# Optimization experiments

Hardware: AMD Instinct MI355X
Metric: run time of the kernel (lower is better)

## Reference

```python
import jax, jax.numpy as jnp
import numpy as np

GAMMA = 1.4
N_PTS, N_IC, HID = 32768, 16384, 128


def _mlp(layers, p):
    # tanh MLP; layers = list of (W, b), last layer linear
    h = p
    for W, b in layers[:-1]:
        h = jnp.tanh(h @ W + b)
    W, b = layers[-1]
    return h @ W + b


def setup_inputs() -> dict:
    key = jax.random.key(0)
    ks = jax.random.split(key, 16)
    d = {
        "x_train": jax.random.uniform(ks[0], (N_PTS, 3), jnp.float32),
        "x_initial": jax.random.uniform(ks[1], (N_IC, 3), jnp.float32),
        "ic": jax.random.uniform(ks[2], (4, 4), jnp.float32),
    }
    def lin(k, fi, fo):
        return jax.random.normal(k, (fi, fo), jnp.float32) * np.float32(np.sqrt(1.0 / fi))
    dims_m = [(3, HID), (HID, HID), (HID, HID), (HID, 4)]
    dims_n = [(3, HID), (HID, HID), (HID, HID), (HID, 1)]
    for i, (fi, fo) in enumerate(dims_m):
        d[f"mw{i}"] = lin(ks[3 + i], fi, fo)
        d[f"mb{i}"] = jnp.zeros((fo,), jnp.float32)
    for i, (fi, fo) in enumerate(dims_n):
        d[f"nw{i}"] = lin(ks[8 + i], fi, fo)
        d[f"nb{i}"] = jnp.zeros((fo,), jnp.float32)
    return d


def _loss(x_train, x_initial, ic,
          mw0, mb0, mw1, mb1, mw2, mb2, mw3, mb3,
          nw0, nb0, nw1, nb1, nw2, nb2, nw3, nb3):
    layers_m = [(mw0, mb0), (mw1, mb1), (mw2, mb2), (mw3, mb3)]
    layers_n = [(nw0, nb0), (nw1, nb1), (nw2, nb2), (nw3, nb3)]

    def prim(p):  # p: (3,) = (x, y, t)
        o = _mlp(layers_m, p)
        rho, pr, u, v = o[0], o[1], o[2], o[3]
        E = pr / (GAMMA - 1.0) + 0.5 * rho * (u * u + v * v)
        return rho, pr, u, v, E

    def Ufn(p):  # conserved state U1..U4
        rho, pr, u, v, E = prim(p)
        return jnp.stack([rho, rho * u, rho * v, E])

    def quant(p):  # [U1..U4, f1..f4, g1..g4]
        rho, pr, u, v, E = prim(p)
        U = jnp.stack([rho, rho * u, rho * v, E])
        f = jnp.stack([rho * u, rho * u * u + pr, rho * u * v, u * (E + pr)])
        g = jnp.stack([rho * v, rho * u * v, rho * v * v + pr, v * (E + pr)])
        return jnp.concatenate([U, f, g])

    # one fused forward-mode Jacobian sweep replaces 20 torch autograd.grad calls
    J = jax.vmap(jax.jacfwd(quant))(x_train)            # (N, 12, 3)
    Hs = jax.vmap(jax.jacfwd(jax.jacfwd(Ufn)))(x_train)  # (N, 4, 3, 3)

    mu = 0.01 * jnp.squeeze(_mlp(layers_n, x_train), -1) ** 2  # (N,)
    lap = Hs[:, :, 0, 0] + Hs[:, :, 1, 1]               # U_xx + U_yy, (N, 4)
    # res_i = U_i_t + f_i_x + g_i_y - mu * (U_i_xx + U_i_yy)
    res = J[:, 0:4, 2] + J[:, 4:8, 0] + J[:, 8:12, 1] - mu[:, None] * lap
    r = jnp.mean(res ** 2, axis=0)                      # (4,) -> r1..r4

    # initial-condition quadrant loss (masked means, jit-safe)
    pred = _mlp(layers_m, x_initial)                    # (Ni, 4)
    xl = x_initial[:, 0] < 0.5
    xr = x_initial[:, 0] > 0.5
    yt = x_initial[:, 1] > 0.5
    yb = x_initial[:, 1] < 0.5
    perm = jnp.array([0, 3, 1, 2])  # ic columns -> [rho, p, u, v] target order
    init_loss = jnp.float32(0.0)
    for row, mask in ((1, xl & yt), (3, xr & yt), (0, xl & yb), (2, xr & yb)):
        tgt = ic[row][perm]                             # (4,)
        m = mask.astype(pred.dtype)
        denom = jnp.maximum(jnp.sum(m), 1.0)
        init_loss = init_loss + jnp.sum(m[:, None] * (pred - tgt) ** 2) / denom

    return jnp.sum(r) + 10.0 * init_loss + 0.1 * jnp.mean(mu ** 2)


def reference(x_train, x_initial, ic,
              mw0, mb0, mw1, mb1, mw2, mb2, mw3, mb3,
              nw0, nb0, nw1, nb1, nw2, nb2, nw3, nb3):
    return _loss(x_train, x_initial, ic,
                 mw0, mb0, mw1, mb1, mw2, mb2, mw3, mb3,
                 nw0, nb0, nw1, nb1, nw2, nb2, nw3, nb3)
```

## Files before the change

kernel.cpp:

```cpp
#include <hip/hip_runtime.h>

#define NPTS 32768
#define NIC  16384
#define GRID 256
#define GRID_MU 512
#define BLK  512
#define NW   8

typedef __attribute__((ext_vector_type(8))) _Float16 f16x8;
typedef __attribute__((ext_vector_type(4))) float f32x4;

#define SWZ(e, r) ((e) ^ (((r) & 7) << 3))
#define MFMA16 __builtin_amdgcn_mfma_f32_16x16x32_f16

__device__ __forceinline__ float tanh_fast(float x) {
    float e = __expf(2.0f * x);
    return 1.0f - 2.0f / (e + 1.0f);
}

__device__ __forceinline__ float wave_allsum(float v) {
#pragma unroll
    for (int off = 32; off > 0; off >>= 1) v += __shfl_xor(v, off, 64);
    return v;
}

__device__ __forceinline__ unsigned short f2hb(float x) {
    return __builtin_bit_cast(unsigned short, (_Float16)x);
}
__device__ __forceinline__ uint2 pack4h(float a, float b, float c, float d) {
    return make_uint2((unsigned)f2hb(a) | ((unsigned)f2hb(b) << 16),
                      (unsigned)f2hb(c) | ((unsigned)f2hb(d) << 16));
}

__global__ __launch_bounds__(BLK) void k_prep(
    const float* __restrict__ mw1, const float* __restrict__ mw2,
    const float* __restrict__ nw1, const float* __restrict__ nw2,
    const float* __restrict__ mw3,
    unsigned short* __restrict__ wt1, unsigned short* __restrict__ wt2,
    unsigned short* __restrict__ nt1, unsigned short* __restrict__ nt2,
    unsigned short* __restrict__ w3t) {
    const int tid = threadIdx.x;
    const int bk = blockIdx.x;
    if (bk == 4) {
        for (int i = tid; i < 2048; i += BLK) w3t[i] = 0;
        __syncthreads();
        if (tid < 512) {
            const int j = tid & 127, k = tid >> 7;
            w3t[k * 128 + SWZ(j, k)] = f2hb(mw3[j * 4 + k]);
        }
        return;
    }
    const float* src = (bk == 0) ? mw1 : (bk == 1) ? mw2 : (bk == 2) ? nw1 : nw2;
    unsigned short* dst = (bk == 0) ? wt1 : (bk == 1) ? wt2 : (bk == 2) ? nt1 : nt2;
    __shared__ float sM[128 * 129];
#pragma unroll
    for (int k = 0; k < 32; k++) {
        const int idx = tid + k * BLK;
        const int j = idx >> 7, n = idx & 127;
        sM[n * 129 + j] = src[idx];
    }
    __syncthreads();
#pragma unroll
    for (int k = 0; k < 32; k++) {
        const int d = tid + k * BLK;
        const int n = d >> 7, js = d & 127;
        const int j = js ^ ((n & 7) << 3);
        dst[d] = f2hb(sM[n * 129 + j]);
    }
}

__global__ __launch_bounds__(BLK) void k_residual(
    const float* __restrict__ xtr,
    const float* __restrict__ mw0, const float* __restrict__ mb0,
    const float* __restrict__ mb1, const float* __restrict__ mb2,
    const float* __restrict__ mb3,
    const unsigned short* __restrict__ wt1, const unsigned short* __restrict__ wt2,
    const unsigned short* __restrict__ w3t,
    const float* __restrict__ muArr, float* __restrict__ resPart) {
    __shared__ __align__(16) _Float16 sW1[16384];
    __shared__ __align__(16) _Float16 sW2[16384];
    __shared__ __align__(16) _Float16 sW3[2048];
    __shared__ __align__(16) _Float16 sH[6 * 4096];
    __shared__ __align__(16) float sO[6 * 32 * 4];
    __shared__ float sB[260];

    const int tid = threadIdx.x;
    const int lane = tid & 63, wv = tid >> 6;
    const int g = lane >> 4, l15 = lane & 15;
    const int rtp = wv >> 1;
    const int ptile = wv & 1;
    const int bp = ptile * 16 + l15;
    const int p32 = tid & 31;
    const int chunk = tid >> 5;

    {
        const uint4* s4 = (const uint4*)wt1;
        uint4* d4 = (uint4*)sW1;
#pragma unroll
        for (int k = 0; k < 4; k++) d4[tid + k * BLK] = s4[tid + k * BLK];
        s4 = (const uint4*)wt2; d4 = (uint4*)sW2;
#pragma unroll
        for (int k = 0; k < 4; k++) d4[tid + k * BLK] = s4[tid + k * BLK];
        if (tid < 256) ((uint4*)sW3)[tid] = ((const uint4*)w3t)[tid];
        if (tid < 128) { sB[tid] = mb1[tid]; sB[128 + tid] = mb2[tid]; }
        if (tid < 4) sB[256 + tid] = mb3[tid];
    }
    float wxr[8], wyr[8], wzr[8], wbr[8];
#pragma unroll
    for (int j = 0; j < 8; j++) {
        const int n = chunk * 8 + j;
        wxr[j] = mw0[n]; wyr[j] = mw0[128 + n]; wzr[j] = mw0[256 + n]; wbr[j] = mb0[n];
    }
    __syncthreads();

    float racc0 = 0.f, racc1 = 0.f, racc2 = 0.f, racc3 = 0.f;
    const int base = blockIdx.x * 128;

    for (int b = 0; b < 4; b++) {
        const int pt0 = base + b * 32;

        {
            const int p = pt0 + p32;
            const float x = xtr[p * 3 + 0], y = xtr[p * 3 + 1], t = xtr[p * 3 + 2];
            float ch[6][8];
#pragma unroll
            for (int j = 0; j < 8; j++) {
                const float z = fmaf(wxr[j], x, fmaf(wyr[j], y, fmaf(wzr[j], t, wbr[j])));
                const float a = tanh_fast(z);
                const float s = 1.f - a * a;
                ch[0][j] = a;
                ch[1][j] = s * wxr[j];
                ch[2][j] = s * wyr[j];
                ch[3][j] = s * wzr[j];
                ch[4][j] = -2.f * a * s * wxr[j] * wxr[j];
                ch[5][j] = -2.f * a * s * wyr[j] * wyr[j];
            }
            const int off = p32 * 128 + SWZ(chunk * 8, p32);
#pragma unroll
            for (int c = 0; c < 6; c++) {
                const uint2 lo = pack4h(ch[c][0], ch[c][1], ch[c][2], ch[c][3]);
                const uint2 hi = pack4h(ch[c][4], ch[c][5], ch[c][6], ch[c][7]);
                *(uint4*)&sH[c * 4096 + off] = make_uint4(lo.x, lo.y, hi.x, hi.y);
            }
        }
        __syncthreads();

#pragma unroll
        for (int L = 0; L < 2; L++) {
            const _Float16* W = (L == 0) ? sW1 : sW2;
            f32x4 acc[2][6];
#pragma unroll
            for (int rr = 0; rr < 2; rr++)
#pragma unroll
                for (int c = 0; c < 6; c++) acc[rr][c] = (f32x4){0.f, 0.f, 0.f, 0.f};
#pragma unroll
            for (int ks = 0; ks < 4; ks++) {
                const int ee = SWZ(ks * 32 + g * 8, l15);
                const f16x8 A0 = *(const f16x8*)&W[(rtp * 32 + l15) * 128 + ee];
                const f16x8 A1 = *(const f16x8*)&W[(rtp * 32 + 16 + l15) * 128 + ee];
#pragma unroll
                for (int c = 0; c < 6; c++) {
                    const f16x8 Bv = *(const f16x8*)&sH[c * 4096 + bp * 128 + ee];
                    acc[0][c] = MFMA16(A0, Bv, acc[0][c], 0, 0, 0);
                    acc[1][c] = MFMA16(A1, Bv, acc[1][c], 0, 0, 0);
                }
            }
            float ch[2][6][4];
#pragma unroll
            for (int rr = 0; rr < 2; rr++)
#pragma unroll
                for (int r = 0; r < 4; r++) {
                    const int n = rtp * 32 + rr * 16 + g * 4 + r;
                    const float z0 = acc[rr][0][r] + sB[L * 128 + n];
                    const float a = tanh_fast(z0);
                    const float s = 1.f - a * a;
                    const float zx = acc[rr][1][r], zy = acc[rr][2][r];
                    ch[rr][0][r] = a;
                    ch[rr][1][r] = s * zx;
                    ch[rr][2][r] = s * zy;
                    ch[rr][3][r] = s * acc[rr][3][r];
                    ch[rr][4][r] = s * acc[rr][4][r] - 2.f * a * s * zx * zx;
                    ch[rr][5][r] = s * acc[rr][5][r] - 2.f * a * s * zy * zy;
                }
            __syncthreads();
#pragma unroll
            for (int rr = 0; rr < 2; rr++) {
                const int eo = bp * 128 + SWZ(rtp * 32 + rr * 16 + g * 4, bp);
#pragma unroll
                for (int c = 0; c < 6; c++)
                    *(uint2*)&sH[c * 4096 + eo] =
                        pack4h(ch[rr][c][0], ch[rr][c][1], ch[rr][c][2], ch[rr][c][3]);
            }
            __syncthreads();
        }

#pragma unroll
        for (int tt = 0; tt < 2; tt++) {
            const int t = wv + tt * 8;
            if (t < 12) {
                const int c = t % 6, pti = t / 6;
                const int fp = pti * 16 + l15;
                f32x4 a4 = (f32x4){0.f, 0.f, 0.f, 0.f};
#pragma unroll
                for (int ks = 0; ks < 4; ks++) {
                    const int ee = SWZ(ks * 32 + g * 8, l15);
                    const f16x8 Af = *(const f16x8*)&sW3[l15 * 128 + ee];
                    const f16x8 Bf = *(const f16x8*)&sH[c * 4096 + fp * 128 + ee];
                    a4 = MFMA16(Af, Bf, a4, 0, 0, 0);
                }
                if (g == 0) {
                    float4 o = make_float4(a4[0], a4[1], a4[2], a4[3]);
                    if (c == 0) { o.x += sB[256]; o.y += sB[257]; o.z += sB[258]; o.w += sB[259]; }
                    *(float4*)&sO[(c * 32 + fp) * 4] = o;
                }
            }
        }
        __syncthreads();

        {
            const float m = muArr[pt0 + p32];
            float oq[4][6];
#pragma unroll
            for (int c = 0; c < 6; c++) {
                const float4 o = *(const float4*)&sO[(c * 32 + p32) * 4];
                oq[0][c] = o.x; oq[1][c] = o.y; oq[2][c] = o.z; oq[3][c] = o.w;
            }
            const float rho = oq[0][0], rho_x = oq[0][1], rho_y = oq[0][2],
                        rho_t = oq[0][3], rho_xx = oq[0][4], rho_yy = oq[0][5];
            const float pr = oq[1][0], pr_x = oq[1][1], pr_y = oq[1][2],
                        pr_t = oq[1][3], pr_xx = oq[1][4], pr_yy = oq[1][5];
            const float u = oq[2][0], u_x = oq[2][1], u_y = oq[2][2],
                        u_t = oq[2][3], u_xx = oq[2][4], u_yy = oq[2][5];
            const float v = oq[3][0], v_x = oq[3][1], v_y = oq[3][2],
                        v_t = oq[3][3], v_xx = oq[3][4], v_yy = oq[3][5];

            const float ig1 = 2.5f;
            const float ke = 0.5f * (u * u + v * v);
            const float E = pr * ig1 + rho * ke;
            const float d_x = u * u_x + v * v_x;
            const float d_y = u * u_y + v * v_y;
            const float d_t = u * u_t + v * v_t;
            const float E_x = pr_x * ig1 + rho_x * ke + rho * d_x;
            const float E_y = pr_y * ig1 + rho_y * ke + rho * d_y;
            const float E_t = pr_t * ig1 + rho_t * ke + rho * d_t;
            const float E_xx = pr_xx * ig1 + rho_xx * ke + 2.f * rho_x * d_x +
                               rho * (u_x * u_x + u * u_xx + v_x * v_x + v * v_xx);
            const float E_yy = pr_yy * ig1 + rho_yy * ke + 2.f * rho_y * d_y +
                               rho * (u_y * u_y + u * u_yy + v_y * v_y + v * v_yy);

            const float r1 = rho_t + (rho_x * u + rho * u_x) + (rho_y * v + rho * v_y)
                           - m * (rho_xx + rho_yy);
            const float r2 = (rho_t * u + rho * u_t)
                           + (rho_x * u * u + 2.f * rho * u * u_x + pr_x)
                           + (rho_y * u * v + rho * u_y * v + rho * u * v_y)
                           - m * ((rho_xx * u + 2.f * rho_x * u_x + rho * u_xx)
                                + (rho_yy * u + 2.f * rho_y * u_y + rho * u_yy));
            const float r3 = (rho_t * v + rho * v_t)
                           + (rho_x * u * v + rho * u_x * v + rho * u * v_x)
                           + (rho_y * v * v + 2.f * rho * v * v_y + pr_y)
                           - m * ((rho_xx * v + 2.f * rho_x * v_x + rho * v_xx)
                                + (rho_yy * v + 2.f * rho_y * v_y + rho * v_yy));
            const float r4 = E_t
                           + (u_x * (E + pr) + u * (E_x + pr_x))
                           + (v_y * (E + pr) + v * (E_y + pr_y))
                           - m * (E_xx + E_yy);
            if (tid < 32) {
                racc0 += r1 * r1; racc1 += r2 * r2;
                racc2 += r3 * r3; racc3 += r4 * r4;
            }
        }
    }

    if (wv == 0) {
        racc0 = wave_allsum(racc0);
        racc1 = wave_allsum(racc1);
        racc2 = wave_allsum(racc2);
        racc3 = wave_allsum(racc3);
        if (lane == 0) {
            resPart[blockIdx.x * 4 + 0] = racc0;
            resPart[blockIdx.x * 4 + 1] = racc1;
            resPart[blockIdx.x * 4 + 2] = racc2;
            resPart[blockIdx.x * 4 + 3] = racc3;
        }
    }
}

__global__ __launch_bounds__(BLK) void k_mu(
    const float* __restrict__ xtr,
    const float* __restrict__ nw0, const float* __restrict__ nb0,
    const float* __restrict__ nb1, const float* __restrict__ nb2,
    const float* __restrict__ nw3, const float* __restrict__ nb3,
    const unsigned short* __restrict__ nt1, const unsigned short* __restrict__ nt2,
    float* __restrict__ muArr, float* __restrict__ muPart) {
    __shared__ __align__(16) _Float16 sW1[16384];
    __shared__ __align__(16) _Float16 sW2[16384];
    __shared__ __align__(16) _Float16 sH[4096];
    __shared__ float sV[128], sB[257];
    __shared__ float sRed[NW];

    const int tid = threadIdx.x;
    const int lane = tid & 63, wv = tid >> 6;
    const int g = lane >> 4, l15 = lane & 15;
    const int rtp = wv >> 1, ptile = wv & 1;
    const int bp = ptile * 16 + l15;
    const int p32 = tid & 31;
    const int chunk = tid >> 5;

    {
        const uint4* s4 = (const uint4*)nt1;
        uint4* d4 = (uint4*)sW1;
#pragma unroll
        for (int k = 0; k < 4; k++) d4[tid + k * BLK] = s4[tid + k * BLK];
        s4 = (const uint4*)nt2; d4 = (uint4*)sW2;
#pragma unroll
        for (int k = 0; k < 4; k++) d4[tid + k * BLK] = s4[tid + k * BLK];
        if (tid < 128) { sV[tid] = nw3[tid]; sB[tid] = nb1[tid]; }
        else if (tid < 256) sB[tid] = nb2[tid - 128];
        if (tid == 256) sB[256] = nb3[0];
    }
    float wxr[8], wyr[8], wzr[8], wbr[8];
#pragma unroll
    for (int j = 0; j < 8; j++) {
        const int n = chunk * 8 + j;
        wxr[j] = nw0[n]; wyr[j] = nw0[128 + n]; wzr[j] = nw0[256 + n]; wbr[j] = nb0[n];
    }
    __syncthreads();

    float accMu2 = 0.f;

    for (int b = 0; b < 2; b++) {
        const int pt0 = blockIdx.x * 64 + b * 32;
        {
            const int p = pt0 + p32;
            const float x = xtr[p * 3 + 0], y = xtr[p * 3 + 1], t = xtr[p * 3 + 2];
            float hv[8];
#pragma unroll
            for (int j = 0; j < 8; j++)
                hv[j] = tanh_fast(fmaf(wxr[j], x, fmaf(wyr[j], y, fmaf(wzr[j], t, wbr[j]))));
            const uint2 lo = pack4h(hv[0], hv[1], hv[2], hv[3]);
            const uint2 hi = pack4h(hv[4], hv[5], hv[6], hv[7]);
            *(uint4*)&sH[p32 * 128 + SWZ(chunk * 8, p32)] = make_uint4(lo.x, lo.y, hi.x, hi.y);
        }
        __syncthreads();
#pragma unroll
        for (int L = 0; L < 2; L++) {
            const _Float16* W = (L == 0) ? sW1 : sW2;
            f32x4 acc[2];
            acc[0] = (f32x4){0.f, 0.f, 0.f, 0.f};
            acc[1] = (f32x4){0.f, 0.f, 0.f, 0.f};
#pragma unroll
            for (int ks = 0; ks < 4; ks++) {
                const int ee = SWZ(ks * 32 + g * 8, l15);
                const f16x8 A0 = *(const f16x8*)&W[(rtp * 32 + l15) * 128 + ee];
                const f16x8 A1 = *(const f16x8*)&W[(rtp * 32 + 16 + l15) * 128 + ee];
                const f16x8 Bv = *(const f16x8*)&sH[bp * 128 + ee];
                acc[0] = MFMA16(A0, Bv, acc[0], 0, 0, 0);
                acc[1] = MFMA16(A1, Bv, acc[1], 0, 0, 0);
            }
            float hv[2][4];
#pragma unroll
            for (int rr = 0; rr < 2; rr++)
#pragma unroll
                for (int r = 0; r < 4; r++) {
                    const int n = rtp * 32 + rr * 16 + g * 4 + r;
                    hv[rr][r] = tanh_fast(acc[rr][r] + sB[L * 128 + n]);
                }
            __syncthreads();
#pragma unroll
            for (int rr = 0; rr < 2; rr++)
                *(uint2*)&sH[bp * 128 + SWZ(rtp * 32 + rr * 16 + g * 4, bp)] =
                    pack4h(hv[rr][0], hv[rr][1], hv[rr][2], hv[rr][3]);
            __syncthreads();
        }
#pragma unroll
        for (int q = 0; q < 4; q++) {
            const int lp = wv * 4 + q;
            const float h1 = (float)sH[lp * 128 + SWZ(lane, lp)];
            const float h2 = (float)sH[lp * 128 + SWZ(64 + lane, lp)];
            float o = fmaf(h1, sV[lane], h2 * sV[64 + lane]);
            o = wave_allsum(o) + sB[256];
            const float muv = 0.01f * o * o;
            if (lane == 0) muArr[pt0 + lp] = muv;
            accMu2 += muv * muv;
        }
        __syncthreads();
    }
    if (lane == 0) sRed[wv] = accMu2;
    __syncthreads();
    if (tid == 0) {
        float s = 0.f;
#pragma unroll
        for (int w = 0; w < NW; w++) s += sRed[w];
        muPart[blockIdx.x] = s;
    }
}

__global__ __launch_bounds__(BLK) void k_ic(
    const float* __restrict__ xin,
    const float* __restrict__ mw0, const float* __restrict__ mb0,
    const float* __restrict__ mb1, const float* __restrict__ mb2,
    const float* __restrict__ mw3, const float* __restrict__ mb3,
    const unsigned short* __restrict__ wt1, const unsigned short* __restrict__ wt2,
    const float* __restrict__ icg, float* __restrict__ icPart) {
    __shared__ __align__(16) _Float16 sW1[16384];
    __shared__ __align__(16) _Float16 sW2[16384];
    __shared__ __align__(16) _Float16 sH[4096];
    __shared__ float sW3v[512];
    __shared__ float sB[260];
    __shared__ float sTq[16];
    __shared__ float sRed[NW][8];

    const int tid = threadIdx.x;
    const int lane = tid & 63, wv = tid >> 6;
    const int g = lane >> 4, l15 = lane & 15;
    const int rtp = wv >> 1, ptile = wv & 1;
    const int bp = ptile * 16 + l15;
    const int p32 = tid & 31;
    const int chunk = tid >> 5;

    {
        const uint4* s4 = (const uint4*)wt1;
        uint4* d4 = (uint4*)sW1;
#pragma unroll
        for (int k = 0; k < 4; k++) d4[tid + k * BLK] = s4[tid + k * BLK];
        s4 = (const uint4*)wt2; d4 = (uint4*)sW2;
#pragma unroll
        for (int k = 0; k < 4; k++) d4[tid + k * BLK] = s4[tid + k * BLK];
        {
            const int k = tid >> 7, j = tid & 127;
            sW3v[k * 128 + j] = mw3[j * 4 + k];
        }
        if (tid < 128) { sB[tid] = mb1[tid]; sB[128 + tid] = mb2[tid]; }
        if (tid < 4) sB[256 + tid] = mb3[tid];
        if (tid < 16) {
            const int k = tid & 3, q = tid >> 2;
            const int row = (q == 0) ? 1 : ((q == 1) ? 3 : ((q == 2) ? 0 : 2));
            const int pc = (k == 0) ? 0 : ((k == 1) ? 3 : ((k == 2) ? 1 : 2));
            sTq[q * 4 + k] = icg[row * 4 + pc];
        }
    }
    float wxr[8], wyr[8], wzr[8], wbr[8];
#pragma unroll
    for (int j = 0; j < 8; j++) {
        const int n = chunk * 8 + j;
        wxr[j] = mw0[n]; wyr[j] = mw0[128 + n]; wzr[j] = mw0[256 + n]; wbr[j] = mb0[n];
    }
    __syncthreads();

    float qs[4] = {0, 0, 0, 0}, qc[4] = {0, 0, 0, 0};

    for (int b = 0; b < 2; b++) {
        const int pt0 = blockIdx.x * 64 + b * 32;
        {
            const int p = pt0 + p32;
            const float x = xin[p * 3 + 0], y = xin[p * 3 + 1], t = xin[p * 3 + 2];
            float hv[8];
#pragma unroll
            for (int j = 0; j < 8; j++)
                hv[j] = tanh_fast(fmaf(wxr[j], x, fmaf(wyr[j], y, fmaf(wzr[j], t, wbr[j]))));
            const uint2 lo = pack4h(hv[0], hv[1], hv[2], hv[3]);
            const uint2 hi = pack4h(hv[4], hv[5], hv[6], hv[7]);
            *(uint4*)&sH[p32 * 128 + SWZ(chunk * 8, p32)] = make_uint4(lo.x, lo.y, hi.x, hi.y);
        }
        __syncthreads();
#pragma unroll
        for (int L = 0; L < 2; L++) {
            const _Float16* W = (L == 0) ? sW1 : sW2;
            f32x4 acc[2];
            acc[0] = (f32x4){0.f, 0.f, 0.f, 0.f};
            acc[1] = (f32x4){0.f, 0.f, 0.f, 0.f};
#pragma unroll
            for (int ks = 0; ks < 4; ks++) {
                const int ee = SWZ(ks * 32 + g * 8, l15);
                const f16x8 A0 = *(const f16x8*)&W[(rtp * 32 + l15) * 128 + ee];
                const f16x8 A1 = *(const f16x8*)&W[(rtp * 32 + 16 + l15) * 128 + ee];
                const f16x8 Bv = *(const f16x8*)&sH[bp * 128 + ee];
                acc[0] = MFMA16(A0, Bv, acc[0], 0, 0, 0);
                acc[1] = MFMA16(A1, Bv, acc[1], 0, 0, 0);
            }
            float hv[2][4];
#pragma unroll
            for (int rr = 0; rr < 2; rr++)
#pragma unroll
                for (int r = 0; r < 4; r++) {
                    const int n = rtp * 32 + rr * 16 + g * 4 + r;
                    hv[rr][r] = tanh_fast(acc[rr][r] + sB[L * 128 + n]);
                }
            __syncthreads();
#pragma unroll
            for (int rr = 0; rr < 2; rr++)
                *(uint2*)&sH[bp * 128 + SWZ(rtp * 32 + rr * 16 + g * 4, bp)] =
                    pack4h(hv[rr][0], hv[rr][1], hv[rr][2], hv[rr][3]);
            __syncthreads();
        }
#pragma unroll
        for (int q = 0; q < 4; q++) {
            const int lp = wv * 4 + q;
            const int p = pt0 + lp;
            const float h1 = (float)sH[lp * 128 + SWZ(lane, lp)];
            const float h2 = (float)sH[lp * 128 + SWZ(64 + lane, lp)];
            float o0 = fmaf(h1, sW3v[lane], h2 * sW3v[64 + lane]);
            float o1 = fmaf(h1, sW3v[128 + lane], h2 * sW3v[192 + lane]);
            float o2 = fmaf(h1, sW3v[256 + lane], h2 * sW3v[320 + lane]);
            float o3 = fmaf(h1, sW3v[384 + lane], h2 * sW3v[448 + lane]);
            o0 = wave_allsum(o0) + sB[256];
            o1 = wave_allsum(o1) + sB[257];
            o2 = wave_allsum(o2) + sB[258];
            o3 = wave_allsum(o3) + sB[259];

            const float x = xin[p * 3 + 0];
            const float y = xin[p * 3 + 1];
            int quad = -1;
            if (x < 0.5f && y > 0.5f) quad = 0;
            else if (x > 0.5f && y > 0.5f) quad = 1;
            else if (x < 0.5f && y < 0.5f) quad = 2;
            else if (x > 0.5f && y < 0.5f) quad = 3;
            if (quad >= 0) {
                const float d0 = o0 - sTq[quad * 4 + 0];
                const float d1 = o1 - sTq[quad * 4 + 1];
                const float d2 = o2 - sTq[quad * 4 + 2];
                const float d3 = o3 - sTq[quad * 4 + 3];
                const float ss = d0 * d0 + d1 * d1 + d2 * d2 + d3 * d3;
#pragma unroll
                for (int qq = 0; qq < 4; qq++) {
                    qs[qq] += (quad == qq) ? ss : 0.f;
                    qc[qq] += (quad == qq) ? 1.f : 0.f;
                }
            }
        }
        __syncthreads();
    }

    if (lane == 0) {
#pragma unroll
        for (int q = 0; q < 4; q++) { sRed[wv][q] = qs[q]; sRed[wv][4 + q] = qc[q]; }
    }
    __syncthreads();
    if (tid == 0) {
        float s[8] = {0, 0, 0, 0, 0, 0, 0, 0};
#pragma unroll
        for (int w = 0; w < NW; w++)
#pragma unroll
            for (int q = 0; q < 8; q++) s[q] += sRed[w][q];
#pragma unroll
        for (int q = 0; q < 8; q++) icPart[blockIdx.x * 8 + q] = s[q];
    }
}

__global__ void k_fin(const float* __restrict__ resPart, const float* __restrict__ muPart,
                      const float* __restrict__ icPart, float* __restrict__ out) {
    const int lane = threadIdx.x;
    float r[4] = {0, 0, 0, 0};
    float m2 = 0.f;
    float qs[4] = {0, 0, 0, 0}, qc[4] = {0, 0, 0, 0};
    for (int b = lane; b < GRID; b += 64) {
#pragma unroll
        for (int i = 0; i < 4; i++) r[i] += resPart[b * 4 + i];
#pragma unroll
        for (int q = 0; q < 4; q++) {
            qs[q] += icPart[b * 8 + q];
            qc[q] += icPart[b * 8 + 4 + q];
        }
    }
    for (int b = lane; b < GRID_MU; b += 64) m2 += muPart[b];
#pragma unroll
    for (int i = 0; i < 4; i++) r[i] = wave_allsum(r[i]);
    m2 = wave_allsum(m2);
#pragma unroll
    for (int q = 0; q < 4; q++) { qs[q] = wave_allsum(qs[q]); qc[q] = wave_allsum(qc[q]); }
    if (lane == 0) {
        const float sumr = (r[0] + r[1] + r[2] + r[3]) / (float)NPTS;
        float init_loss = 0.f;
#pragma unroll
        for (int q = 0; q < 4; q++) init_loss += qs[q] / fmaxf(qc[q], 1.f);
        out[0] = sumr + 10.f * init_loss + 0.1f * (m2 / (float)NPTS);
    }
}

extern "C" void kernel_launch(void* const* d_in, const int* in_sizes, int n_in,
                              void* d_out, int out_size, void* d_ws, size_t ws_size,
                              hipStream_t stream) {
    const float* xtr = (const float*)d_in[0];
    const float* xin = (const float*)d_in[1];
    const float* icg = (const float*)d_in[2];
    const float* mw0 = (const float*)d_in[3];
    const float* mb0 = (const float*)d_in[4];
    const float* mw1 = (const float*)d_in[5];
    const float* mb1 = (const float*)d_in[6];
    const float* mw2 = (const float*)d_in[7];
    const float* mb2 = (const float*)d_in[8];
    const float* mw3 = (const float*)d_in[9];
    const float* mb3 = (const float*)d_in[10];
    const float* nw0 = (const float*)d_in[11];
    const float* nb0 = (const float*)d_in[12];
    const float* nw1 = (const float*)d_in[13];
    const float* nb1 = (const float*)d_in[14];
    const float* nw2 = (const float*)d_in[15];
    const float* nb2 = (const float*)d_in[16];
    const float* nw3 = (const float*)d_in[17];
    const float* nb3 = (const float*)d_in[18];

    float* wsf = (float*)d_ws;
    float* muArr = wsf;
    float* resPart = wsf + 32768;
    float* muPart = wsf + 33792;
    float* icPart = wsf + 34304;
    unsigned short* wt1 = (unsigned short*)(wsf + 36864);
    unsigned short* wt2 = wt1 + 16384;
    unsigned short* nt1 = wt2 + 16384;
    unsigned short* nt2 = nt1 + 16384;
    unsigned short* w3t = nt2 + 16384;

    k_prep<<<5, BLK, 0, stream>>>(mw1, mw2, nw1, nw2, mw3, wt1, wt2, nt1, nt2, w3t);
    k_mu<<<GRID_MU, BLK, 0, stream>>>(xtr, nw0, nb0, nb1, nb2, nw3, nb3, nt1, nt2,
                                      muArr, muPart);
    k_ic<<<GRID, BLK, 0, stream>>>(xin, mw0, mb0, mb1, mb2, mw3, mb3, wt1, wt2,
                                   icg, icPart);
    k_residual<<<GRID, BLK, 0, stream>>>(xtr, mw0, mb0, mb1, mb2, mb3,
                                         wt1, wt2, w3t, muArr, resPart);
    k_fin<<<1, 64, 0, stream>>>(resPart, muPart, icPart, (float*)d_out);
}
```

Measured before the change: 68.69 us.

## Fuse mu, initial-condition, and residual kernels into one per-block kernel

```diff
diff --git a/kernel.cpp b/kernel.cpp
--- a/kernel.cpp
+++ b/kernel.cpp
@@ -3,7 +3,6 @@
 #define NPTS 32768
 #define NIC  16384
 #define GRID 256
-#define GRID_MU 512
 #define BLK  512
 #define NW   8
 
@@ -69,29 +68,129 @@
     }
 }
 
-__global__ __launch_bounds__(BLK) void k_residual(
-    const float* __restrict__ xtr,
+__global__ __launch_bounds__(BLK) void k_fused(
+    const float* __restrict__ xtr, const float* __restrict__ xin,
+    const float* __restrict__ icg,
     const float* __restrict__ mw0, const float* __restrict__ mb0,
     const float* __restrict__ mb1, const float* __restrict__ mb2,
-    const float* __restrict__ mb3,
+    const float* __restrict__ mw3, const float* __restrict__ mb3,
+    const float* __restrict__ nw0, const float* __restrict__ nb0,
+    const float* __restrict__ nb1, const float* __restrict__ nb2,
+    const float* __restrict__ nw3, const float* __restrict__ nb3,
     const unsigned short* __restrict__ wt1, const unsigned short* __restrict__ wt2,
+    const unsigned short* __restrict__ nt1, const unsigned short* __restrict__ nt2,
     const unsigned short* __restrict__ w3t,
-    const float* __restrict__ muArr, float* __restrict__ resPart) {
+    float* __restrict__ resPart, float* __restrict__ muPart,
+    float* __restrict__ icPart) {
     __shared__ __align__(16) _Float16 sW1[16384];
     __shared__ __align__(16) _Float16 sW2[16384];
+    __shared__ __align__(16) _Float16 sH[6 * 4096];
     __shared__ __align__(16) _Float16 sW3[2048];
-    __shared__ __align__(16) _Float16 sH[6 * 4096];
-    __shared__ __align__(16) float sO[6 * 32 * 4];
-    __shared__ float sB[260];
+    __shared__ __align__(16) float sO[768];
+    __shared__ float sB[520];
+    __shared__ float sV[128];
+    __shared__ float sW3v[512];
+    __shared__ float sMu[128];
+    __shared__ float sTq[16];
+    __shared__ float sRed[NW][8];
 
     const int tid = threadIdx.x;
     const int lane = tid & 63, wv = tid >> 6;
     const int g = lane >> 4, l15 = lane & 15;
-    const int rtp = wv >> 1;
-    const int ptile = wv & 1;
+    const int rtp = wv >> 1, ptile = wv & 1;
     const int bp = ptile * 16 + l15;
     const int p32 = tid & 31;
     const int chunk = tid >> 5;
+    const int base = blockIdx.x * 128;
+
+    {
+        const uint4* s4 = (const uint4*)nt1;
+        uint4* d4 = (uint4*)sW1;
+#pragma unroll
+        for (int k = 0; k < 4; k++) d4[tid + k * BLK] = s4[tid + k * BLK];
+        s4 = (const uint4*)nt2; d4 = (uint4*)sW2;
+#pragma unroll
+        for (int k = 0; k < 4; k++) d4[tid + k * BLK] = s4[tid + k * BLK];
+        if (tid < 128) {
+            sV[tid] = nw3[tid];
+            sB[260 + tid] = nb1[tid];
+            sB[388 + tid] = nb2[tid];
+        }
+        if (tid == 0) sB[516] = nb3[0];
+    }
+    float wxr[8], wyr[8], wzr[8], wbr[8];
+#pragma unroll
+    for (int j = 0; j < 8; j++) {
+        const int n = chunk * 8 + j;
+        wxr[j] = nw0[n]; wyr[j] = nw0[128 + n]; wzr[j] = nw0[256 + n]; wbr[j] = nb0[n];
+    }
+    __syncthreads();
+
+    float accMu2 = 0.f;
+    for (int b = 0; b < 4; b++) {
+        const int pt0 = base + b * 32;
+        {
+            const int p = pt0 + p32;
+            const float x = xtr[p * 3 + 0], y = xtr[p * 3 + 1], t = xtr[p * 3 + 2];
+            float hv[8];
+#pragma unroll
+            for (int j = 0; j < 8; j++)
+                hv[j] = tanh_fast(fmaf(wxr[j], x, fmaf(wyr[j], y, fmaf(wzr[j], t, wbr[j]))));
+            const uint2 lo = pack4h(hv[0], hv[1], hv[2], hv[3]);
+            const uint2 hi = pack4h(hv[4], hv[5], hv[6], hv[7]);
+            *(uint4*)&sH[p32 * 128 + SWZ(chunk * 8, p32)] = make_uint4(lo.x, lo.y, hi.x, hi.y);
+        }
+        __syncthreads();
+#pragma unroll
+        for (int L = 0; L < 2; L++) {
+            const _Float16* W = (L == 0) ? sW1 : sW2;
+            f32x4 a0 = (f32x4){0.f, 0.f, 0.f, 0.f};
+            f32x4 a1 = (f32x4){0.f, 0.f, 0.f, 0.f};
+#pragma unroll
+            for (int ks = 0; ks < 4; ks++) {
+                const int ee = SWZ(ks * 32 + g * 8, l15);
+                const f16x8 A0 = *(const f16x8*)&W[(rtp * 32 + l15) * 128 + ee];
+                const f16x8 A1 = *(const f16x8*)&W[(rtp * 32 + 16 + l15) * 128 + ee];
+                const f16x8 Bv = *(const f16x8*)&sH[bp * 128 + ee];
+                a0 = MFMA16(A0, Bv, a0, 0, 0, 0);
+                a1 = MFMA16(A1, Bv, a1, 0, 0, 0);
+            }
+            float hv[2][4];
+#pragma unroll
+            for (int r = 0; r < 4; r++) {
+                const int n0 = rtp * 32 + g * 4 + r;
+                hv[0][r] = tanh_fast(a0[r] + sB[260 + L * 128 + n0]);
+                hv[1][r] = tanh_fast(a1[r] + sB[260 + L * 128 + n0 + 16]);
+            }
+            __syncthreads();
+#pragma unroll
+            for (int rr = 0; rr < 2; rr++)
+                *(uint2*)&sH[bp * 128 + SWZ(rtp * 32 + rr * 16 + g * 4, bp)] =
+                    pack4h(hv[rr][0], hv[rr][1], hv[rr][2], hv[rr][3]);
+            __syncthreads();
+        }
+#pragma unroll
+        for (int q = 0; q < 4; q++) {
+            const int lp = wv * 4 + q;
+            const float h1 = (float)sH[lp * 128 + SWZ(lane, lp)];
+            const float h2 = (float)sH[lp * 128 + SWZ(64 + lane, lp)];
+            float o = fmaf(h1, sV[lane], h2 * sV[64 + lane]);
+            o = wave_allsum(o) + sB[516];
+            const float muv = 0.01f * o * o;
+            if (lane == 0) sMu[b * 32 + lp] = muv;
+            accMu2 += muv * muv;
+        }
+        __syncthreads();
+    }
+    if (lane == 0) sRed[wv][0] = accMu2;
+    __syncthreads();
+    if (tid == 0) {
+        float s = 0.f;
+#pragma unroll
+        for (int w = 0; w < NW; w++) s += sRed[w][0];
+        muPart[blockIdx.x] = s;
+    }
+    __syncthreads();
 
     {
         const uint4* s4 = (const uint4*)wt1;
@@ -102,10 +201,19 @@
 #pragma unroll
         for (int k = 0; k < 4; k++) d4[tid + k * BLK] = s4[tid + k * BLK];
         if (tid < 256) ((uint4*)sW3)[tid] = ((const uint4*)w3t)[tid];
+        {
+            const int k = tid >> 7, j = tid & 127;
+            sW3v[k * 128 + j] = mw3[j * 4 + k];
+        }
         if (tid < 128) { sB[tid] = mb1[tid]; sB[128 + tid] = mb2[tid]; }
         if (tid < 4) sB[256 + tid] = mb3[tid];
-    }
-    float wxr[8], wyr[8], wzr[8], wbr[8];
+        if (tid < 16) {
+            const int k = tid & 3, q = tid >> 2;
+            const int row = (q == 0) ? 1 : ((q == 1) ? 3 : ((q == 2) ? 0 : 2));
+            const int pc = (k == 0) ? 0 : ((k == 1) ? 3 : ((k == 2) ? 1 : 2));
+            sTq[q * 4 + k] = icg[row * 4 + pc];
+        }
+    }
 #pragma unroll
     for (int j = 0; j < 8; j++) {
         const int n = chunk * 8 + j;
@@ -113,9 +221,103 @@
     }
     __syncthreads();
 
+    float qs[4] = {0, 0, 0, 0}, qc[4] = {0, 0, 0, 0};
+    for (int b = 0; b < 2; b++) {
+        const int pt0 = blockIdx.x * 64 + b * 32;
+        {
+            const int p = pt0 + p32;
+            const float x = xin[p * 3 + 0], y = xin[p * 3 + 1], t = xin[p * 3 + 2];
+            float hv[8];
+#pragma unroll
+            for (int j = 0; j < 8; j++)
+                hv[j] = tanh_fast(fmaf(wxr[j], x, fmaf(wyr[j], y, fmaf(wzr[j], t, wbr[j]))));
+            const uint2 lo = pack4h(hv[0], hv[1], hv[2], hv[3]);
+            const uint2 hi = pack4h(hv[4], hv[5], hv[6], hv[7]);
+            *(uint4*)&sH[p32 * 128 + SWZ(chunk * 8, p32)] = make_uint4(lo.x, lo.y, hi.x, hi.y);
+        }
+        __syncthreads();
+#pragma unroll
+        for (int L = 0; L < 2; L++) {
+            const _Float16* W = (L == 0) ? sW1 : sW2;
+            f32x4 a0 = (f32x4){0.f, 0.f, 0.f, 0.f};
+            f32x4 a1 = (f32x4){0.f, 0.f, 0.f, 0.f};
+#pragma unroll
+            for (int ks = 0; ks < 4; ks++) {
+                const int ee = SWZ(ks * 32 + g * 8, l15);
+                const f16x8 A0 = *(const f16x8*)&W[(rtp * 32 + l15) * 128 + ee];
+                const f16x8 A1 = *(const f16x8*)&W[(rtp * 32 + 16 + l15) * 128 + ee];
+                const f16x8 Bv = *(const f16x8*)&sH[bp * 128 + ee];
+                a0 = MFMA16(A0, Bv, a0, 0, 0, 0);
+                a1 = MFMA16(A1, Bv, a1, 0, 0, 0);
+            }
+            float hv[2][4];
+#pragma unroll
+            for (int r = 0; r < 4; r++) {
+                const int n0 = rtp * 32 + g * 4 + r;
+                hv[0][r] = tanh_fast(a0[r] + sB[L * 128 + n0]);
+                hv[1][r] = tanh_fast(a1[r] + sB[L * 128 + n0 + 16]);
+            }
+            __syncthreads();
+#pragma unroll
+            for (int rr = 0; rr < 2; rr++)
+                *(uint2*)&sH[bp * 128 + SWZ(rtp * 32 + rr * 16 + g * 4, bp)] =
+                    pack4h(hv[rr][0], hv[rr][1], hv[rr][2], hv[rr][3]);
+            __syncthreads();
+        }
+#pragma unroll
+        for (int q = 0; q < 4; q++) {
+            const int lp = wv * 4 + q;
+            const int p = pt0 + lp;
+            const float h1 = (float)sH[lp * 128 + SWZ(lane, lp)];
+            const float h2 = (float)sH[lp * 128 + SWZ(64 + lane, lp)];
+            float o0 = fmaf(h1, sW3v[lane], h2 * sW3v[64 + lane]);
+            float o1 = fmaf(h1, sW3v[128 + lane], h2 * sW3v[192 + lane]);
+            float o2 = fmaf(h1, sW3v[256 + lane], h2 * sW3v[320 + lane]);
+            float o3 = fmaf(h1, sW3v[384 + lane], h2 * sW3v[448 + lane]);
+            o0 = wave_allsum(o0) + sB[256];
+            o1 = wave_allsum(o1) + sB[257];
+            o2 = wave_allsum(o2) + sB[258];
+            o3 = wave_allsum(o3) + sB[259];
+
+            const float x = xin[p * 3 + 0];
+            const float y = xin[p * 3 + 1];
+            int quad = -1;
+            if (x < 0.5f && y > 0.5f) quad = 0;
+            else if (x > 0.5f && y > 0.5f) quad = 1;
+            else if (x < 0.5f && y < 0.5f) quad = 2;
+            else if (x > 0.5f && y < 0.5f) quad = 3;
+            if (quad >= 0) {
+                const float d0 = o0 - sTq[quad * 4 + 0];
+                const float d1 = o1 - sTq[quad * 4 + 1];
+                const float d2 = o2 - sTq[quad * 4 + 2];
+                const float d3 = o3 - sTq[quad * 4 + 3];
+                const float ss = d0 * d0 + d1 * d1 + d2 * d2 + d3 * d3;
+#pragma unroll
+                for (int qq = 0; qq < 4; qq++) {
+                    qs[qq] += (quad == qq) ? ss : 0.f;
+                    qc[qq] += (quad == qq) ? 1.f : 0.f;
+                }
+            }
+        }
+        __syncthreads();
+    }
+    if (lane == 0) {
+#pragma unroll
+        for (int q = 0; q < 4; q++) { sRed[wv][q] = qs[q]; sRed[wv][4 + q] = qc[q]; }
+    }
+    __syncthreads();
+    if (tid == 0) {
+        float s[8] = {0, 0, 0, 0, 0, 0, 0, 0};
+#pragma unroll
+        for (int w = 0; w < NW; w++)
+#pragma unroll
+            for (int q = 0; q < 8; q++) s[q] += sRed[w][q];
+#pragma unroll
+        for (int q = 0; q < 8; q++) icPart[blockIdx.x * 8 + q] = s[q];
+    }
+    __syncthreads();
+
     float racc0 = 0.f, racc1 = 0.f, racc2 = 0.f, racc3 = 0.f;
-    const int base = blockIdx.x * 128;
-
     for (int b = 0; b < 4; b++) {
         const int pt0 = base + b * 32;
 
@@ -218,7 +420,7 @@
         __syncthreads();
 
         {
-            const float m = muArr[pt0 + p32];
+            const float m = sMu[b * 32 + p32];
             float oq[4][6];
 #pragma unroll
             for (int c = 0; c < 6; c++) {
@@ -269,6 +471,7 @@
                 racc2 += r3 * r3; racc3 += r4 * r4;
             }
         }
+        __syncthreads();
     }
 
     if (wv == 0) {
@@ -285,268 +488,6 @@
     }
 }
 
-__global__ __launch_bounds__(BLK) void k_mu(
-    const float* __restrict__ xtr,
-    const float* __restrict__ nw0, const float* __restrict__ nb0,
-    const float* __restrict__ nb1, const float* __restrict__ nb2,
-    const float* __restrict__ nw3, const float* __restrict__ nb3,
-    const unsigned short* __restrict__ nt1, const unsigned short* __restrict__ nt2,
-    float* __restrict__ muArr, float* __restrict__ muPart) {
-    __shared__ __align__(16) _Float16 sW1[16384];
-    __shared__ __align__(16) _Float16 sW2[16384];
-    __shared__ __align__(16) _Float16 sH[4096];
-    __shared__ float sV[128], sB[257];
-    __shared__ float sRed[NW];
-
-    const int tid = threadIdx.x;
-    const int lane = tid & 63, wv = tid >> 6;
-    const int g = lane >> 4, l15 = lane & 15;
-    const int rtp = wv >> 1, ptile = wv & 1;
-    const int bp = ptile * 16 + l15;
-    const int p32 = tid & 31;
-    const int chunk = tid >> 5;
-
-    {
-        const uint4* s4 = (const uint4*)nt1;
-        uint4* d4 = (uint4*)sW1;
-#pragma unroll
-        for (int k = 0; k < 4; k++) d4[tid + k * BLK] = s4[tid + k * BLK];
-        s4 = (const uint4*)nt2; d4 = (uint4*)sW2;
-#pragma unroll
-        for (int k = 0; k < 4; k++) d4[tid + k * BLK] = s4[tid + k * BLK];
-        if (tid < 128) { sV[tid] = nw3[tid]; sB[tid] = nb1[tid]; }
-        else if (tid < 256) sB[tid] = nb2[tid - 128];
-        if (tid == 256) sB[256] = nb3[0];
-    }
-    float wxr[8], wyr[8], wzr[8], wbr[8];
-#pragma unroll
-    for (int j = 0; j < 8; j++) {
-        const int n = chunk * 8 + j;
-        wxr[j] = nw0[n]; wyr[j] = nw0[128 + n]; wzr[j] = nw0[256 + n]; wbr[j] = nb0[n];
-    }
-    __syncthreads();
-
-    float accMu2 = 0.f;
-
-    for (int b = 0; b < 2; b++) {
-        const int pt0 = blockIdx.x * 64 + b * 32;
-        {
-            const int p = pt0 + p32;
-            const float x = xtr[p * 3 + 0], y = xtr[p * 3 + 1], t = xtr[p * 3 + 2];
-            float hv[8];
-#pragma unroll
-            for (int j = 0; j < 8; j++)
-                hv[j] = tanh_fast(fmaf(wxr[j], x, fmaf(wyr[j], y, fmaf(wzr[j], t, wbr[j]))));
-            const uint2 lo = pack4h(hv[0], hv[1], hv[2], hv[3]);
-            const uint2 hi = pack4h(hv[4], hv[5], hv[6], hv[7]);
-            *(uint4*)&sH[p32 * 128 + SWZ(chunk * 8, p32)] = make_uint4(lo.x, lo.y, hi.x, hi.y);
-        }
-        __syncthreads();
-#pragma unroll
-        for (int L = 0; L < 2; L++) {
-            const _Float16* W = (L == 0) ? sW1 : sW2;
-            f32x4 acc[2];
-            acc[0] = (f32x4){0.f, 0.f, 0.f, 0.f};
-            acc[1] = (f32x4){0.f, 0.f, 0.f, 0.f};
-#pragma unroll
-            for (int ks = 0; ks < 4; ks++) {
-                const int ee = SWZ(ks * 32 + g * 8, l15);
-                const f16x8 A0 = *(const f16x8*)&W[(rtp * 32 + l15) * 128 + ee];
-                const f16x8 A1 = *(const f16x8*)&W[(rtp * 32 + 16 + l15) * 128 + ee];
-                const f16x8 Bv = *(const f16x8*)&sH[bp * 128 + ee];
-                acc[0] = MFMA16(A0, Bv, acc[0], 0, 0, 0);
-                acc[1] = MFMA16(A1, Bv, acc[1], 0, 0, 0);
-            }
-            float hv[2][4];
-#pragma unroll
-            for (int rr = 0; rr < 2; rr++)
-#pragma unroll
-                for (int r = 0; r < 4; r++) {
-                    const int n = rtp * 32 + rr * 16 + g * 4 + r;
-                    hv[rr][r] = tanh_fast(acc[rr][r] + sB[L * 128 + n]);
-                }
-            __syncthreads();
-#pragma unroll
-            for (int rr = 0; rr < 2; rr++)
-                *(uint2*)&sH[bp * 128 + SWZ(rtp * 32 + rr * 16 + g * 4, bp)] =
-                    pack4h(hv[rr][0], hv[rr][1], hv[rr][2], hv[rr][3]);
-            __syncthreads();
-        }
-#pragma unroll
-        for (int q = 0; q < 4; q++) {
-            const int lp = wv * 4 + q;
-            const float h1 = (float)sH[lp * 128 + SWZ(lane, lp)];
-            const float h2 = (float)sH[lp * 128 + SWZ(64 + lane, lp)];
-            float o = fmaf(h1, sV[lane], h2 * sV[64 + lane]);
-            o = wave_allsum(o) + sB[256];
-            const float muv = 0.01f * o * o;
-            if (lane == 0) muArr[pt0 + lp] = muv;
-            accMu2 += muv * muv;
-        }
-        __syncthreads();
-    }
-    if (lane == 0) sRed[wv] = accMu2;
-    __syncthreads();
-    if (tid == 0) {
-        float s = 0.f;
-#pragma unroll
-        for (int w = 0; w < NW; w++) s += sRed[w];
-        muPart[blockIdx.x] = s;
-    }
-}
-
-__global__ __launch_bounds__(BLK) void k_ic(
-    const float* __restrict__ xin,
-    const float* __restrict__ mw0, const float* __restrict__ mb0,
-    const float* __restrict__ mb1, const float* __restrict__ mb2,
-    const float* __restrict__ mw3, const float* __restrict__ mb3,
-    const unsigned short* __restrict__ wt1, const unsigned short* __restrict__ wt2,
-    const float* __restrict__ icg, float* __restrict__ icPart) {
-    __shared__ __align__(16) _Float16 sW1[16384];
-    __shared__ __align__(16) _Float16 sW2[16384];
-    __shared__ __align__(16) _Float16 sH[4096];
-    __shared__ float sW3v[512];
-    __shared__ float sB[260];
-    __shared__ float sTq[16];
-    __shared__ float sRed[NW][8];
-
-    const int tid = threadIdx.x;
-    const int lane = tid & 63, wv = tid >> 6;
-    const int g = lane >> 4, l15 = lane & 15;
-    const int rtp = wv >> 1, ptile = wv & 1;
-    const int bp = ptile * 16 + l15;
-    const int p32 = tid & 31;
-    const int chunk = tid >> 5;
-
-    {
-        const uint4* s4 = (const uint4*)wt1;
-        uint4* d4 = (uint4*)sW1;
-#pragma unroll
-        for (int k = 0; k < 4; k++) d4[tid + k * BLK] = s4[tid + k * BLK];
-        s4 = (const uint4*)wt2; d4 = (uint4*)sW2;
-#pragma unroll
-        for (int k = 0; k < 4; k++) d4[tid + k * BLK] = s4[tid + k * BLK];
-        {
-            const int k = tid >> 7, j = tid & 127;
-            sW3v[k * 128 + j] = mw3[j * 4 + k];
-        }
-        if (tid < 128) { sB[tid] = mb1[tid]; sB[128 + tid] = mb2[tid]; }
-        if (tid < 4) sB[256 + tid] = mb3[tid];
-        if (tid < 16) {
-            const int k = tid & 3, q = tid >> 2;
-            const int row = (q == 0) ? 1 : ((q == 1) ? 3 : ((q == 2) ? 0 : 2));
-            const int pc = (k == 0) ? 0 : ((k == 1) ? 3 : ((k == 2) ? 1 : 2));
-            sTq[q * 4 + k] = icg[row * 4 + pc];
-        }
-    }
-    float wxr[8], wyr[8], wzr[8], wbr[8];
-#pragma unroll
-    for (int j = 0; j < 8; j++) {
-        const int n = chunk * 8 + j;
-        wxr[j] = mw0[n]; wyr[j] = mw0[128 + n]; wzr[j] = mw0[256 + n]; wbr[j] = mb0[n];
-    }
-    __syncthreads();
-
-    float qs[4] = {0, 0, 0, 0}, qc[4] = {0, 0, 0, 0};
-
-    for (int b = 0; b < 2; b++) {
-        const int pt0 = blockIdx.x * 64 + b * 32;
-        {
-            const int p = pt0 + p32;
-            const float x = xin[p * 3 + 0], y = xin[p * 3 + 1], t = xin[p * 3 + 2];
-            float hv[8];
-#pragma unroll
-            for (int j = 0; j < 8; j++)
-                hv[j] = tanh_fast(fmaf(wxr[j], x, fmaf(wyr[j], y, fmaf(wzr[j], t, wbr[j]))));
-            const uint2 lo = pack4h(hv[0], hv[1], hv[2], hv[3]);
-            const uint2 hi = pack4h(hv[4], hv[5], hv[6], hv[7]);
-            *(uint4*)&sH[p32 * 128 + SWZ(chunk * 8, p32)] = make_uint4(lo.x, lo.y, hi.x, hi.y);
-        }
-        __syncthreads();
-#pragma unroll
-        for (int L = 0; L < 2; L++) {
-            const _Float16* W = (L == 0) ? sW1 : sW2;
-            f32x4 acc[2];
-            acc[0] = (f32x4){0.f, 0.f, 0.f, 0.f};
-            acc[1] = (f32x4){0.f, 0.f, 0.f, 0.f};
-#pragma unroll
-            for (int ks = 0; ks < 4; ks++) {
-                const int ee = SWZ(ks * 32 + g * 8, l15);
-                const f16x8 A0 = *(const f16x8*)&W[(rtp * 32 + l15) * 128 + ee];
-                const f16x8 A1 = *(const f16x8*)&W[(rtp * 32 + 16 + l15) * 128 + ee];
-                const f16x8 Bv = *(const f16x8*)&sH[bp * 128 + ee];
-                acc[0] = MFMA16(A0, Bv, acc[0], 0, 0, 0);
-                acc[1] = MFMA16(A1, Bv, acc[1], 0, 0, 0);
-            }
-            float hv[2][4];
-#pragma unroll
-            for (int rr = 0; rr < 2; rr++)
-#pragma unroll
-                for (int r = 0; r < 4; r++) {
-                    const int n = rtp * 32 + rr * 16 + g * 4 + r;
-                    hv[rr][r] = tanh_fast(acc[rr][r] + sB[L * 128 + n]);
-                }
-            __syncthreads();
-#pragma unroll
-            for (int rr = 0; rr < 2; rr++)
-                *(uint2*)&sH[bp * 128 + SWZ(rtp * 32 + rr * 16 + g * 4, bp)] =
-                    pack4h(hv[rr][0], hv[rr][1], hv[rr][2], hv[rr][3]);
-            __syncthreads();
-        }
-#pragma unroll
-        for (int q = 0; q < 4; q++) {
-            const int lp = wv * 4 + q;
-            const int p = pt0 + lp;
-            const float h1 = (float)sH[lp * 128 + SWZ(lane, lp)];
-            const float h2 = (float)sH[lp * 128 + SWZ(64 + lane, lp)];
-            float o0 = fmaf(h1, sW3v[lane], h2 * sW3v[64 + lane]);
-            float o1 = fmaf(h1, sW3v[128 + lane], h2 * sW3v[192 + lane]);
-            float o2 = fmaf(h1, sW3v[256 + lane], h2 * sW3v[320 + lane]);
-            float o3 = fmaf(h1, sW3v[384 + lane], h2 * sW3v[448 + lane]);
-            o0 = wave_allsum(o0) + sB[256];
-            o1 = wave_allsum(o1) + sB[257];
-            o2 = wave_allsum(o2) + sB[258];
-            o3 = wave_allsum(o3) + sB[259];
-
-            const float x = xin[p * 3 + 0];
-            const float y = xin[p * 3 + 1];
-            int quad = -1;
-            if (x < 0.5f && y > 0.5f) quad = 0;
-            else if (x > 0.5f && y > 0.5f) quad = 1;
-            else if (x < 0.5f && y < 0.5f) quad = 2;
-            else if (x > 0.5f && y < 0.5f) quad = 3;
-            if (quad >= 0) {
-                const float d0 = o0 - sTq[quad * 4 + 0];
-                const float d1 = o1 - sTq[quad * 4 + 1];
-                const float d2 = o2 - sTq[quad * 4 + 2];
-                const float d3 = o3 - sTq[quad * 4 + 3];
-                const float ss = d0 * d0 + d1 * d1 + d2 * d2 + d3 * d3;
-#pragma unroll
-                for (int qq = 0; qq < 4; qq++) {
-                    qs[qq] += (quad == qq) ? ss : 0.f;
-                    qc[qq] += (quad == qq) ? 1.f : 0.f;
-                }
-            }
-        }
-        __syncthreads();
-    }
-
-    if (lane == 0) {
-#pragma unroll
-        for (int q = 0; q < 4; q++) { sRed[wv][q] = qs[q]; sRed[wv][4 + q] = qc[q]; }
-    }
-    __syncthreads();
-    if (tid == 0) {
-        float s[8] = {0, 0, 0, 0, 0, 0, 0, 0};
-#pragma unroll
-        for (int w = 0; w < NW; w++)
-#pragma unroll
-            for (int q = 0; q < 8; q++) s[q] += sRed[w][q];
-#pragma unroll
-        for (int q = 0; q < 8; q++) icPart[blockIdx.x * 8 + q] = s[q];
-    }
-}
-
 __global__ void k_fin(const float* __restrict__ resPart, const float* __restrict__ muPart,
                       const float* __restrict__ icPart, float* __restrict__ out) {
     const int lane = threadIdx.x;
@@ -556,13 +497,13 @@
     for (int b = lane; b < GRID; b += 64) {
 #pragma unroll
         for (int i = 0; i < 4; i++) r[i] += resPart[b * 4 + i];
+        m2 += muPart[b];
 #pragma unroll
         for (int q = 0; q < 4; q++) {
             qs[q] += icPart[b * 8 + q];
             qc[q] += icPart[b * 8 + 4 + q];
         }
     }
-    for (int b = lane; b < GRID_MU; b += 64) m2 += muPart[b];
 #pragma unroll
     for (int i = 0; i < 4; i++) r[i] = wave_allsum(r[i]);
     m2 = wave_allsum(m2);
@@ -601,22 +542,20 @@
     const float* nb3 = (const float*)d_in[18];
 
     float* wsf = (float*)d_ws;
-    float* muArr = wsf;
-    float* resPart = wsf + 32768;
-    float* muPart = wsf + 33792;
-    float* icPart = wsf + 34304;
-    unsigned short* wt1 = (unsigned short*)(wsf + 36864);
+    float* resPart = wsf;
+    float* muPart = wsf + 1024;
+    float* icPart = wsf + 1280;
+    unsigned short* wt1 = (unsigned short*)(wsf + 3328);
     unsigned short* wt2 = wt1 + 16384;
     unsigned short* nt1 = wt2 + 16384;
     unsigned short* nt2 = nt1 + 16384;
     unsigned short* w3t = nt2 + 16384;
 
     k_prep<<<5, BLK, 0, stream>>>(mw1, mw2, nw1, nw2, mw3, wt1, wt2, nt1, nt2, w3t);
-    k_mu<<<GRID_MU, BLK, 0, stream>>>(xtr, nw0, nb0, nb1, nb2, nw3, nb3, nt1, nt2,
-                                      muArr, muPart);
-    k_ic<<<GRID, BLK, 0, stream>>>(xin, mw0, mb0, mb1, mb2, mw3, mb3, wt1, wt2,
-                                   icg, icPart);
-    k_residual<<<GRID, BLK, 0, stream>>>(xtr, mw0, mb0, mb1, mb2, mb3,
-                                         wt1, wt2, w3t, muArr, resPart);
+    k_fused<<<GRID, BLK, 0, stream>>>(xtr, xin, icg,
+                                      mw0, mb0, mb1, mb2, mw3, mb3,
+                                      nw0, nb0, nb1, nb2, nw3, nb3,
+                                      wt1, wt2, nt1, nt2, w3t,
+                                      resPart, muPart, icPart);
     k_fin<<<1, 64, 0, stream>>>(resPart, muPart, icPart, (float*)d_out);
 }
```

Result: faster. 66.95 us (-2.5%).
